# Kernel optimization log

Measured on AMD Instinct MI355X. Metric: run time of the kernel, lower is better.

## Reference

```python
import jax, jax.numpy as jnp
import numpy as np


def _build_affine_mat(affine, scale, translate, shear):
    """Replicates the torch stacking exactly: torch.stack(cols, dim=2) makes each
    stacked 3-vector a COLUMN of the 3x3 matrix."""
    tx, ty, tz = affine[:, 0], affine[:, 1], affine[:, 2]
    sx, sy, sz = scale[:, 0], scale[:, 1], scale[:, 2]
    trx, try_, trz = translate[:, 0], translate[:, 1], translate[:, 2]
    sh_xy, sh_xz, sh_yx, sh_yz, sh_zx, sh_zy = (shear[:, i] for i in range(6))
    one = jnp.ones_like(tx)
    zero = jnp.zeros_like(tx)

    col = lambda a, b, c: jnp.stack([a, b, c], axis=1)          # [N,3]
    mat3 = lambda c0, c1, c2: jnp.stack([c0, c1, c2], axis=2)   # columns -> [N,3,3]

    rot_x = mat3(col(one, zero, zero),
                 col(zero, jnp.cos(tx), -jnp.sin(tx)),
                 col(zero, jnp.sin(tx), jnp.cos(tx)))
    rot_y = mat3(col(jnp.cos(ty), zero, jnp.sin(ty)),
                 col(zero, one, zero),
                 col(-jnp.sin(ty), zero, jnp.cos(ty)))
    rot_z = mat3(col(jnp.cos(tz), -jnp.sin(tz), zero),
                 col(jnp.sin(tz), jnp.cos(tz), zero),
                 col(zero, zero, one))
    scale_mat = mat3(col(sx, zero, zero), col(zero, sy, zero), col(zero, zero, sz))
    shear_mat = mat3(col(one, jnp.tan(sh_xy), jnp.tan(sh_xz)),
                     col(jnp.tan(sh_yx), one, jnp.tan(sh_yz)),
                     col(jnp.tan(sh_zx), jnp.tan(sh_zy), one))
    trans = jnp.stack([trx, try_, trz], axis=1)[:, :, None]     # [N,3,1]

    m = shear_mat @ (scale_mat @ (rot_z @ (rot_y @ rot_x)))     # [N,3,3]
    return jnp.concatenate([m, trans], axis=-1)                 # [N,3,4]


def _affine_grid_3d(mat, D, H, W):
    """F.affine_grid(mat, [N,C,D,H,W], align_corners=True): grid[n,d,h,w] =
    mat @ (x_w, y_h, z_d, 1), coords in torch (x,y,z) = (W,H,D) order."""
    xs = jnp.linspace(-1.0, 1.0, W)
    ys = jnp.linspace(-1.0, 1.0, H)
    zs = jnp.linspace(-1.0, 1.0, D)
    zz, yy, xx = jnp.meshgrid(zs, ys, xs, indexing='ij')        # each [D,H,W]
    base = jnp.stack([xx, yy, zz], axis=-1)                     # [D,H,W,3]
    grid = jnp.einsum('dhwj,nij->ndhwi', base, mat[:, :, :3])
    return grid + mat[:, None, None, None, :, 3]                # [N,D,H,W,3]


def _grid_sample_3d(src, grid):
    """F.grid_sample(src, grid, mode='bilinear', padding_mode='zeros',
    align_corners=True) for 5-D input."""
    N, C, D, H, W = src.shape
    x, y, z = grid[..., 0], grid[..., 1], grid[..., 2]
    ix = (x + 1.0) * 0.5 * (W - 1)
    iy = (y + 1.0) * 0.5 * (H - 1)
    iz = (z + 1.0) * 0.5 * (D - 1)
    fx, fy, fz = jnp.floor(ix), jnp.floor(iy), jnp.floor(iz)
    wx, wy, wz = ix - fx, iy - fy, iz - fz                      # frac weights
    x0, y0, z0 = fx.astype(jnp.int32), fy.astype(jnp.int32), fz.astype(jnp.int32)

    gather = jax.vmap(lambda im, zi, yi, xi: im[:, zi, yi, xi])  # [C,D,H,W] per batch

    out = jnp.zeros((N, C, D, H, W), dtype=src.dtype)
    for dz in (0, 1):
        for dy in (0, 1):
            for dx in (0, 1):
                xi, yi, zi = x0 + dx, y0 + dy, z0 + dz
                w = ((wx if dx else 1.0 - wx) *
                     (wy if dy else 1.0 - wy) *
                     (wz if dz else 1.0 - wz))
                valid = ((xi >= 0) & (xi < W) & (yi >= 0) & (yi < H) &
                         (zi >= 0) & (zi < D))
                xc = jnp.clip(xi, 0, W - 1)
                yc = jnp.clip(yi, 0, H - 1)
                zc = jnp.clip(zi, 0, D - 1)
                g = gather(src, zc, yc, xc)                      # [N,C,D,H,W]
                out = out + (w * valid)[:, None] * g
    return out


def setup_inputs() -> dict:
    key = jax.random.key(0)
    k = jax.random.split(key, 5)
    N, C, D, H, W = 2, 1, 160, 192, 160
    src = jax.random.normal(k[0], (N, C, D, H, W), dtype=jnp.float32)
    affine = 0.1 * jax.random.normal(k[1], (N, 3), dtype=jnp.float32)
    scale = 1.0 + 0.05 * jax.random.normal(k[2], (N, 3), dtype=jnp.float32)
    translate = 0.05 * jax.random.normal(k[3], (N, 3), dtype=jnp.float32)
    shear = 0.05 * jax.random.normal(k[4], (N, 6), dtype=jnp.float32)
    return {"src": src, "affine": affine, "scale": scale,
            "translate": translate, "shear": shear}


def reference(src, affine, scale, translate, shear):
    mat = _build_affine_mat(affine, scale, translate, shear)     # [N,3,4]
    N, C, D, H, W = src.shape
    grid = _affine_grid_3d(mat, D, H, W)                         # [N,D,H,W,3]
    out = _grid_sample_3d(src, grid)                             # [N,C,D,H,W]
    return out, mat
```

## Files before the change

kernel.cpp:

```cpp
#include <hip/hip_runtime.h>
#include <math.h>

#define N_ 2
#define C_ 1
#define D_ 160
#define H_ 192
#define W_ 160
#define DHW_ (D_*H_*W_)
#define TOTAL_ (N_*DHW_)
#define BLOCKS_PER_N_ (DHW_/256)

__device__ __forceinline__ void matmul3(const float A[3][3], const float B[3][3], float C[3][3]) {
    #pragma unroll
    for (int i = 0; i < 3; ++i)
        #pragma unroll
        for (int j = 0; j < 3; ++j)
            C[i][j] = A[i][0]*B[0][j] + A[i][1]*B[1][j] + A[i][2]*B[2][j];
}

__global__ void build_mat_kernel(const float* __restrict__ affine,
                                 const float* __restrict__ scale,
                                 const float* __restrict__ translate,
                                 const float* __restrict__ shear,
                                 float* __restrict__ mat_out) {
    int n = threadIdx.x;
    if (n >= N_) return;
    float tx = affine[n*3+0], ty = affine[n*3+1], tz = affine[n*3+2];
    float sx = scale[n*3+0],  sy = scale[n*3+1],  sz = scale[n*3+2];
    float t_xy = tanf(shear[n*6+0]), t_xz = tanf(shear[n*6+1]);
    float t_yx = tanf(shear[n*6+2]), t_yz = tanf(shear[n*6+3]);
    float t_zx = tanf(shear[n*6+4]), t_zy = tanf(shear[n*6+5]);
    float cx = cosf(tx), sxv = sinf(tx);
    float cy = cosf(ty), syv = sinf(ty);
    float cz = cosf(tz), szv = sinf(tz);
    float RX[3][3] = {{1,0,0},{0,cx,sxv},{0,-sxv,cx}};
    float RY[3][3] = {{cy,0,-syv},{0,1,0},{syv,0,cy}};
    float RZ[3][3] = {{cz,szv,0},{-szv,cz,0},{0,0,1}};
    float SC[3][3] = {{sx,0,0},{0,sy,0},{0,0,sz}};
    float SH[3][3] = {{1,t_yx,t_zx},{t_xy,1,t_zy},{t_xz,t_yz,1}};
    float M1[3][3], M2[3][3], M3[3][3], M4[3][3];
    matmul3(RY, RX, M1);
    matmul3(RZ, M1, M2);
    matmul3(SC, M2, M3);
    matmul3(SH, M3, M4);
    #pragma unroll
    for (int i = 0; i < 3; ++i) {
        #pragma unroll
        for (int j = 0; j < 3; ++j)
            mat_out[n*12 + i*4 + j] = M4[i][j];
        mat_out[n*12 + i*4 + 3] = translate[n*3 + i];
    }
}

__global__ __launch_bounds__(256)
void affine_sample_kernel(const float* __restrict__ src,
                          const float* __restrict__ mat,
                          float* __restrict__ out) {
    int n     = blockIdx.x / BLOCKS_PER_N_;
    int local = (blockIdx.x % BLOCKS_PER_N_) * 256 + threadIdx.x;

    int w = local % W_;
    int t = local / W_;
    int h = t % H_;
    int d = t / H_;

    const float* m = mat + n * 12;

    float x = -1.0f + w * (2.0f / (W_ - 1));
    float y = -1.0f + h * (2.0f / (H_ - 1));
    float z = -1.0f + d * (2.0f / (D_ - 1));

    float gx = m[0]*x + m[1]*y + m[2]*z  + m[3];
    float gy = m[4]*x + m[5]*y + m[6]*z  + m[7];
    float gz = m[8]*x + m[9]*y + m[10]*z + m[11];

    float ix = (gx + 1.0f) * 0.5f * (W_ - 1);
    float iy = (gy + 1.0f) * 0.5f * (H_ - 1);
    float iz = (gz + 1.0f) * 0.5f * (D_ - 1);

    float fx = floorf(ix), fy = floorf(iy), fz = floorf(iz);
    float wx = ix - fx, wy = iy - fy, wz = iz - fz;
    int x0 = (int)fx, y0 = (int)fy, z0 = (int)fz;

    const float* s = src + n * DHW_;
    float acc = 0.0f;
    #pragma unroll
    for (int dz = 0; dz < 2; ++dz) {
        int  zi  = z0 + dz;
        bool vz  = (zi >= 0) & (zi < D_);
        int  zc  = min(max(zi, 0), D_ - 1);
        float wzz = dz ? wz : 1.0f - wz;
        #pragma unroll
        for (int dy = 0; dy < 2; ++dy) {
            int  yi  = y0 + dy;
            bool vzy = vz & (yi >= 0) & (yi < H_);
            int  yc  = min(max(yi, 0), H_ - 1);
            float wzy = wzz * (dy ? wy : 1.0f - wy);
            int rowoff = (zc * H_ + yc) * W_;
            #pragma unroll
            for (int dx = 0; dx < 2; ++dx) {
                int  xi = x0 + dx;
                bool v  = vzy & (xi >= 0) & (xi < W_);
                int  xc = min(max(xi, 0), W_ - 1);
                float ww = wzy * (dx ? wx : 1.0f - wx);
                float val = v ? s[rowoff + xc] : 0.0f;
                acc += ww * val;
            }
        }
    }
    out[n * DHW_ + local] = acc;
}

extern "C" void kernel_launch(void* const* d_in, const int* in_sizes, int n_in,
                              void* d_out, int out_size, void* d_ws, size_t ws_size,
                              hipStream_t stream) {
    const float* src       = (const float*)d_in[0];
    const float* affine    = (const float*)d_in[1];
    const float* scale     = (const float*)d_in[2];
    const float* translate = (const float*)d_in[3];
    const float* shear     = (const float*)d_in[4];

    float* out     = (float*)d_out;
    float* mat_out = out + TOTAL_;

    build_mat_kernel<<<1, 64, 0, stream>>>(affine, scale, translate, shear, mat_out);
    affine_sample_kernel<<<N_ * BLOCKS_PER_N_, 256, 0, stream>>>(src, mat_out, out);
}
```

Before: 148.6 us.

## Process four voxels per thread with interior fast path and XCD-aware block swizzle

Each thread now computes four consecutive output voxels, hoisting the y/z part of the affine transform and storing results with one float4 write. A wave-uniform fast path skips per-corner bounds checks and clamps when every voxel's eight neighbours are in range, using lerp-form trilinear interpolation. Block IDs are remapped so consecutive work chunks land on the same XCD, which is meant to improve L2 locality of the gathered source reads. Register pressure rises, and boundary waves still run the slow masked path.

```diff
diff --git a/kernel.cpp b/kernel.cpp
--- a/kernel.cpp
+++ b/kernel.cpp
@@ -2,13 +2,18 @@
 #include <math.h>
 
 #define N_ 2
-#define C_ 1
 #define D_ 160
 #define H_ 192
 #define W_ 160
+#define HW_ (H_*W_)
 #define DHW_ (D_*H_*W_)
 #define TOTAL_ (N_*DHW_)
-#define BLOCKS_PER_N_ (DHW_/256)
+#define VPT_ 4
+#define BLK_ 256
+#define ELEMS_PER_BLK_ (BLK_*VPT_)
+#define BLOCKS_PER_N_ (DHW_/ELEMS_PER_BLK_)
+#define NWG_ (TOTAL_/ELEMS_PER_BLK_)
+#define NXCD_ 8
 
 __device__ __forceinline__ void matmul3(const float A[3][3], const float B[3][3], float C[3][3]) {
     #pragma unroll
@@ -56,59 +61,100 @@
 void affine_sample_kernel(const float* __restrict__ src,
                           const float* __restrict__ mat,
                           float* __restrict__ out) {
-    int n     = blockIdx.x / BLOCKS_PER_N_;
-    int local = (blockIdx.x % BLOCKS_PER_N_) * 256 + threadIdx.x;
+    int bid = blockIdx.x;
+    int swz = (bid & (NXCD_-1)) * (NWG_/NXCD_) + (bid >> 3);
 
-    int w = local % W_;
-    int t = local / W_;
-    int h = t % H_;
-    int d = t / H_;
+    int n  = swz / BLOCKS_PER_N_;
+    int lb = (swz % BLOCKS_PER_N_) * ELEMS_PER_BLK_ + threadIdx.x * VPT_;
+
+    int w0 = lb % W_;
+    int t  = lb / W_;
+    int h  = t % H_;
+    int d  = t / H_;
 
     const float* m = mat + n * 12;
-
-    float x = -1.0f + w * (2.0f / (W_ - 1));
     float y = -1.0f + h * (2.0f / (H_ - 1));
     float z = -1.0f + d * (2.0f / (D_ - 1));
+    float byx = m[1]*y + m[2]*z  + m[3];
+    float byy = m[5]*y + m[6]*z  + m[7];
+    float byz = m[9]*y + m[10]*z + m[11];
 
-    float gx = m[0]*x + m[1]*y + m[2]*z  + m[3];
-    float gy = m[4]*x + m[5]*y + m[6]*z  + m[7];
-    float gz = m[8]*x + m[9]*y + m[10]*z + m[11];
-
-    float ix = (gx + 1.0f) * 0.5f * (W_ - 1);
-    float iy = (gy + 1.0f) * 0.5f * (H_ - 1);
-    float iz = (gz + 1.0f) * 0.5f * (D_ - 1);
-
-    float fx = floorf(ix), fy = floorf(iy), fz = floorf(iz);
-    float wx = ix - fx, wy = iy - fy, wz = iz - fz;
-    int x0 = (int)fx, y0 = (int)fy, z0 = (int)fz;
+    int   x0[VPT_], y0[VPT_], z0[VPT_], off[VPT_];
+    float wx[VPT_], wy[VPT_], wz[VPT_];
+    bool  allin = true;
+    #pragma unroll
+    for (int k = 0; k < VPT_; ++k) {
+        float x  = -1.0f + (w0 + k) * (2.0f / (W_ - 1));
+        float ix = (m[0]*x + byx + 1.0f) * 0.5f * (W_ - 1);
+        float iy = (m[4]*x + byy + 1.0f) * 0.5f * (H_ - 1);
+        float iz = (m[8]*x + byz + 1.0f) * 0.5f * (D_ - 1);
+        float fx = floorf(ix), fy = floorf(iy), fz = floorf(iz);
+        wx[k] = ix - fx; wy[k] = iy - fy; wz[k] = iz - fz;
+        x0[k] = (int)fx; y0[k] = (int)fy; z0[k] = (int)fz;
+        off[k] = (z0[k] * H_ + y0[k]) * W_ + x0[k];
+        allin &= ((unsigned)x0[k] < (unsigned)(W_-1)) &
+                 ((unsigned)y0[k] < (unsigned)(H_-1)) &
+                 ((unsigned)z0[k] < (unsigned)(D_-1));
+    }
 
     const float* s = src + n * DHW_;
-    float acc = 0.0f;
-    #pragma unroll
-    for (int dz = 0; dz < 2; ++dz) {
-        int  zi  = z0 + dz;
-        bool vz  = (zi >= 0) & (zi < D_);
-        int  zc  = min(max(zi, 0), D_ - 1);
-        float wzz = dz ? wz : 1.0f - wz;
+    float res[VPT_];
+
+    if (__all(allin)) {
+        float v000[VPT_], v001[VPT_], v010[VPT_], v011[VPT_];
+        float v100[VPT_], v101[VPT_], v110[VPT_], v111[VPT_];
         #pragma unroll
-        for (int dy = 0; dy < 2; ++dy) {
-            int  yi  = y0 + dy;
-            bool vzy = vz & (yi >= 0) & (yi < H_);
-            int  yc  = min(max(yi, 0), H_ - 1);
-            float wzy = wzz * (dy ? wy : 1.0f - wy);
-            int rowoff = (zc * H_ + yc) * W_;
+        for (int k = 0; k < VPT_; ++k) {
+            const float* p = s + off[k];
+            v000[k] = p[0];        v001[k] = p[1];
+            v010[k] = p[W_];       v011[k] = p[W_ + 1];
+            v100[k] = p[HW_];      v101[k] = p[HW_ + 1];
+            v110[k] = p[HW_ + W_]; v111[k] = p[HW_ + W_ + 1];
+        }
+        #pragma unroll
+        for (int k = 0; k < VPT_; ++k) {
+            float c00 = v000[k] + wx[k] * (v001[k] - v000[k]);
+            float c01 = v010[k] + wx[k] * (v011[k] - v010[k]);
+            float c10 = v100[k] + wx[k] * (v101[k] - v100[k]);
+            float c11 = v110[k] + wx[k] * (v111[k] - v110[k]);
+            float c0  = c00 + wy[k] * (c01 - c00);
+            float c1  = c10 + wy[k] * (c11 - c10);
+            res[k] = c0 + wz[k] * (c1 - c0);
+        }
+    } else {
+        #pragma unroll
+        for (int k = 0; k < VPT_; ++k) {
+            float acc = 0.0f;
             #pragma unroll
-            for (int dx = 0; dx < 2; ++dx) {
-                int  xi = x0 + dx;
-                bool v  = vzy & (xi >= 0) & (xi < W_);
-                int  xc = min(max(xi, 0), W_ - 1);
-                float ww = wzy * (dx ? wx : 1.0f - wx);
-                float val = v ? s[rowoff + xc] : 0.0f;
-                acc += ww * val;
+            for (int dz = 0; dz < 2; ++dz) {
+                int  zi  = z0[k] + dz;
+                bool vz  = (zi >= 0) & (zi < D_);
+                int  zc  = min(max(zi, 0), D_ - 1);
+                float wzz = dz ? wz[k] : 1.0f - wz[k];
+                #pragma unroll
+                for (int dy = 0; dy < 2; ++dy) {
+                    int  yi  = y0[k] + dy;
+                    bool vzy = vz & (yi >= 0) & (yi < H_);
+                    int  yc  = min(max(yi, 0), H_ - 1);
+                    float wzy = wzz * (dy ? wy[k] : 1.0f - wy[k]);
+                    int rowoff = (zc * H_ + yc) * W_;
+                    #pragma unroll
+                    for (int dx = 0; dx < 2; ++dx) {
+                        int  xi = x0[k] + dx;
+                        bool v  = vzy & (xi >= 0) & (xi < W_);
+                        int  xc = min(max(xi, 0), W_ - 1);
+                        float ww = wzy * (dx ? wx[k] : 1.0f - wx[k]);
+                        float val = v ? s[rowoff + xc] : 0.0f;
+                        acc += ww * val;
+                    }
+                }
             }
+            res[k] = acc;
         }
     }
-    out[n * DHW_ + local] = acc;
+
+    float4 o = make_float4(res[0], res[1], res[2], res[3]);
+    *reinterpret_cast<float4*>(out + n * DHW_ + lb) = o;
 }
 
 extern "C" void kernel_launch(void* const* d_in, const int* in_sizes, int n_in,
@@ -124,5 +170,5 @@
     float* mat_out = out + TOTAL_;
 
     build_mat_kernel<<<1, 64, 0, stream>>>(affine, scale, translate, shear, mat_out);
-    affine_sample_kernel<<<N_ * BLOCKS_PER_N_, 256, 0, stream>>>(src, mat_out, out);
+    affine_sample_kernel<<<NWG_, BLK_, 0, stream>>>(src, mat_out, out);
 }
```

Result: slower. 201.0 us (+35.2%).

## Fuse matrix build into sampler, two depth slices per thread, XCD-aware block swizzle

Applied to the files above, without the earlier changes.

Drops the separate matrix-building kernel. Each block now computes the 3x4 affine matrix into shared memory, and block 0 writes both matrices to the output. Each thread handles two adjacent depth slices, issues all 16 gathers before doing any arithmetic, and uses branchless mask-multiplied lerps. Block indices are remapped so that consecutive work lands on the same XCD, which is meant to improve L2 locality. The cost is redundant transcendental math per block and higher register pressure.

```diff
diff --git a/kernel.cpp b/kernel.cpp
--- a/kernel.cpp
+++ b/kernel.cpp
@@ -2,13 +2,18 @@
 #include <math.h>
 
 #define N_ 2
-#define C_ 1
 #define D_ 160
 #define H_ 192
 #define W_ 160
+#define HW_ (H_*W_)
 #define DHW_ (D_*H_*W_)
 #define TOTAL_ (N_*DHW_)
-#define BLOCKS_PER_N_ (DHW_/256)
+#define BLK_ 256
+#define BLOCKS_PER_SLAB_ (HW_/BLK_)
+#define PAIRS_ (D_/2)
+#define BLOCKS_PER_N_ (PAIRS_*BLOCKS_PER_SLAB_)
+#define NWG_ (N_*BLOCKS_PER_N_)
+#define NXCD_ 8
 
 __device__ __forceinline__ void matmul3(const float A[3][3], const float B[3][3], float C[3][3]) {
     #pragma unroll
@@ -18,13 +23,10 @@
             C[i][j] = A[i][0]*B[0][j] + A[i][1]*B[1][j] + A[i][2]*B[2][j];
 }
 
-__global__ void build_mat_kernel(const float* __restrict__ affine,
-                                 const float* __restrict__ scale,
-                                 const float* __restrict__ translate,
-                                 const float* __restrict__ shear,
-                                 float* __restrict__ mat_out) {
-    int n = threadIdx.x;
-    if (n >= N_) return;
+__device__ __forceinline__ void compute_mat(int n,
+        const float* __restrict__ affine, const float* __restrict__ scale,
+        const float* __restrict__ translate, const float* __restrict__ shear,
+        float M[12]) {
     float tx = affine[n*3+0], ty = affine[n*3+1], tz = affine[n*3+2];
     float sx = scale[n*3+0],  sy = scale[n*3+1],  sz = scale[n*3+2];
     float t_xy = tanf(shear[n*6+0]), t_xz = tanf(shear[n*6+1]);
@@ -47,68 +49,120 @@
     for (int i = 0; i < 3; ++i) {
         #pragma unroll
         for (int j = 0; j < 3; ++j)
-            mat_out[n*12 + i*4 + j] = M4[i][j];
-        mat_out[n*12 + i*4 + 3] = translate[n*3 + i];
+            M[i*4+j] = M4[i][j];
+        M[i*4+3] = translate[n*3+i];
     }
 }
 
 __global__ __launch_bounds__(256)
 void affine_sample_kernel(const float* __restrict__ src,
-                          const float* __restrict__ mat,
-                          float* __restrict__ out) {
-    int n     = blockIdx.x / BLOCKS_PER_N_;
-    int local = (blockIdx.x % BLOCKS_PER_N_) * 256 + threadIdx.x;
+                          const float* __restrict__ affine,
+                          const float* __restrict__ scale,
+                          const float* __restrict__ translate,
+                          const float* __restrict__ shear,
+                          float* __restrict__ out,
+                          float* __restrict__ mat_out) {
+    int bid = blockIdx.x;
+    int swz = (bid & (NXCD_-1)) * (NWG_/NXCD_) + (bid >> 3);
 
-    int w = local % W_;
-    int t = local / W_;
-    int h = t % H_;
-    int d = t / H_;
+    int n = swz / BLOCKS_PER_N_;
+    int r = swz % BLOCKS_PER_N_;
 
-    const float* m = mat + n * 12;
+    __shared__ float sm[12];
+    if (threadIdx.x == 0) {
+        float M[12];
+        compute_mat(n, affine, scale, translate, shear, M);
+        #pragma unroll
+        for (int i = 0; i < 12; ++i) sm[i] = M[i];
+        if (bid == 0) {
+            #pragma unroll
+            for (int i = 0; i < 12; ++i) mat_out[i] = M[i];
+        }
+    }
+    if (bid == 0 && threadIdx.x == 1) {
+        float M[12];
+        compute_mat(1, affine, scale, translate, shear, M);
+        #pragma unroll
+        for (int i = 0; i < 12; ++i) mat_out[12 + i] = M[i];
+    }
+    __syncthreads();
 
-    float x = -1.0f + w * (2.0f / (W_ - 1));
-    float y = -1.0f + h * (2.0f / (H_ - 1));
-    float z = -1.0f + d * (2.0f / (D_ - 1));
+    int d0  = 2 * (r / BLOCKS_PER_SLAB_);
+    int idx = (r % BLOCKS_PER_SLAB_) * BLK_ + threadIdx.x;
+    int w = idx % W_;
+    int h = idx / W_;
 
-    float gx = m[0]*x + m[1]*y + m[2]*z  + m[3];
-    float gy = m[4]*x + m[5]*y + m[6]*z  + m[7];
-    float gz = m[8]*x + m[9]*y + m[10]*z + m[11];
+    float x = -1.0f + w  * (2.0f / (W_ - 1));
+    float y = -1.0f + h  * (2.0f / (H_ - 1));
+    float z = -1.0f + d0 * (2.0f / (D_ - 1));
 
-    float ix = (gx + 1.0f) * 0.5f * (W_ - 1);
-    float iy = (gy + 1.0f) * 0.5f * (H_ - 1);
-    float iz = (gz + 1.0f) * 0.5f * (D_ - 1);
+    float gx = sm[0]*x + sm[1]*y + sm[2]*z  + sm[3];
+    float gy = sm[4]*x + sm[5]*y + sm[6]*z  + sm[7];
+    float gz = sm[8]*x + sm[9]*y + sm[10]*z + sm[11];
 
-    float fx = floorf(ix), fy = floorf(iy), fz = floorf(iz);
-    float wx = ix - fx, wy = iy - fy, wz = iz - fz;
-    int x0 = (int)fx, y0 = (int)fy, z0 = (int)fz;
+    float ix[2], iy[2], iz[2];
+    ix[0] = (gx + 1.0f) * (0.5f * (W_ - 1));
+    iy[0] = (gy + 1.0f) * (0.5f * (H_ - 1));
+    iz[0] = (gz + 1.0f) * (0.5f * (D_ - 1));
+    const float zs = 2.0f / (D_ - 1);
+    ix[1] = ix[0] + sm[2]  * zs * (0.5f * (W_ - 1));
+    iy[1] = iy[0] + sm[6]  * zs * (0.5f * (H_ - 1));
+    iz[1] = iz[0] + sm[10] * zs * (0.5f * (D_ - 1));
+
+    float wxa[2], wya[2], wza[2];
+    float mx0[2], mx1[2], my0[2], my1[2], mz0[2], mz1[2];
+    int   r00[2], r01[2], r10[2], r11[2], xa0[2], xa1[2];
+    #pragma unroll
+    for (int k = 0; k < 2; ++k) {
+        float fx = floorf(ix[k]), fy = floorf(iy[k]), fz = floorf(iz[k]);
+        wxa[k] = ix[k] - fx; wya[k] = iy[k] - fy; wza[k] = iz[k] - fz;
+        int x0 = (int)fx, y0 = (int)fy, z0 = (int)fz;
+        int x1 = x0 + 1,  y1 = y0 + 1,  z1 = z0 + 1;
+        mx0[k] = ((unsigned)x0 < (unsigned)W_) ? 1.0f : 0.0f;
+        mx1[k] = ((unsigned)x1 < (unsigned)W_) ? 1.0f : 0.0f;
+        my0[k] = ((unsigned)y0 < (unsigned)H_) ? 1.0f : 0.0f;
+        my1[k] = ((unsigned)y1 < (unsigned)H_) ? 1.0f : 0.0f;
+        mz0[k] = ((unsigned)z0 < (unsigned)D_) ? 1.0f : 0.0f;
+        mz1[k] = ((unsigned)z1 < (unsigned)D_) ? 1.0f : 0.0f;
+        int xc0 = min(max(x0, 0), W_-1), xc1 = min(max(x1, 0), W_-1);
+        int yc0 = min(max(y0, 0), H_-1), yc1 = min(max(y1, 0), H_-1);
+        int zc0 = min(max(z0, 0), D_-1), zc1 = min(max(z1, 0), D_-1);
+        r00[k] = (zc0 * H_ + yc0) * W_;
+        r01[k] = (zc0 * H_ + yc1) * W_;
+        r10[k] = (zc1 * H_ + yc0) * W_;
+        r11[k] = (zc1 * H_ + yc1) * W_;
+        xa0[k] = xc0; xa1[k] = xc1;
+    }
 
     const float* s = src + n * DHW_;
-    float acc = 0.0f;
+    float v000[2], v001[2], v010[2], v011[2], v100[2], v101[2], v110[2], v111[2];
     #pragma unroll
-    for (int dz = 0; dz < 2; ++dz) {
-        int  zi  = z0 + dz;
-        bool vz  = (zi >= 0) & (zi < D_);
-        int  zc  = min(max(zi, 0), D_ - 1);
-        float wzz = dz ? wz : 1.0f - wz;
-        #pragma unroll
-        for (int dy = 0; dy < 2; ++dy) {
-            int  yi  = y0 + dy;
-            bool vzy = vz & (yi >= 0) & (yi < H_);
-            int  yc  = min(max(yi, 0), H_ - 1);
-            float wzy = wzz * (dy ? wy : 1.0f - wy);
-            int rowoff = (zc * H_ + yc) * W_;
-            #pragma unroll
-            for (int dx = 0; dx < 2; ++dx) {
-                int  xi = x0 + dx;
-                bool v  = vzy & (xi >= 0) & (xi < W_);
-                int  xc = min(max(xi, 0), W_ - 1);
-                float ww = wzy * (dx ? wx : 1.0f - wx);
-                float val = v ? s[rowoff + xc] : 0.0f;
-                acc += ww * val;
-            }
-        }
+    for (int k = 0; k < 2; ++k) {
+        v000[k] = s[r00[k] + xa0[k]]; v001[k] = s[r00[k] + xa1[k]];
+        v010[k] = s[r01[k] + xa0[k]]; v011[k] = s[r01[k] + xa1[k]];
+        v100[k] = s[r10[k] + xa0[k]]; v101[k] = s[r10[k] + xa1[k]];
+        v110[k] = s[r11[k] + xa0[k]]; v111[k] = s[r11[k] + xa1[k]];
     }
-    out[n * DHW_ + local] = acc;
+
+    float res[2];
+    #pragma unroll
+    for (int k = 0; k < 2; ++k) {
+        float a, b, c00, c01, c10, c11, c0, c1;
+        a = v000[k]*mx0[k]; b = v001[k]*mx1[k]; c00 = a + wxa[k]*(b - a);
+        a = v010[k]*mx0[k]; b = v011[k]*mx1[k]; c01 = a + wxa[k]*(b - a);
+        a = v100[k]*mx0[k]; b = v101[k]*mx1[k]; c10 = a + wxa[k]*(b - a);
+        a = v110[k]*mx0[k]; b = v111[k]*mx1[k]; c11 = a + wxa[k]*(b - a);
+        c00 *= my0[k]; c01 *= my1[k];
+        c10 *= my0[k]; c11 *= my1[k];
+        c0 = c00 + wya[k]*(c01 - c00);
+        c1 = c10 + wya[k]*(c11 - c10);
+        c0 *= mz0[k]; c1 *= mz1[k];
+        res[k] = c0 + wza[k]*(c1 - c0);
+    }
+
+    int obase = n * DHW_ + d0 * HW_ + idx;
+    out[obase]       = res[0];
+    out[obase + HW_] = res[1];
 }
 
 extern "C" void kernel_launch(void* const* d_in, const int* in_sizes, int n_in,
@@ -123,6 +177,6 @@
     float* out     = (float*)d_out;
     float* mat_out = out + TOTAL_;
 
-    build_mat_kernel<<<1, 64, 0, stream>>>(affine, scale, translate, shear, mat_out);
-    affine_sample_kernel<<<N_ * BLOCKS_PER_N_, 256, 0, stream>>>(src, mat_out, out);
+    affine_sample_kernel<<<NWG_, BLK_, 0, stream>>>(src, affine, scale, translate,
+                                                    shear, out, mat_out);
 }
```

Result: slower. 159.2 us (+7.1%).

## Swizzle blocks across XCDs and use branchless paired-load trilinear gather

Applied to the files above, without the earlier changes.

Remaps block IDs so that consecutive blocks land on the same XCD, which should improve L2 locality of the gathered source voxels on MI355X's multi-XCD layout. Replaces the predicated eight-way gather with four row pointers built from a clamped x base. Each row is read with two unconditional inline-asm global loads at offsets 0 and 4 bytes. Out-of-range taps are handled by select and mask multiplies, and the interpolation becomes a lerp chain. This removes branches and per-tap address math, but always loads from the clamped memory location and forces a full vmcnt(0) wait inside the asm.

```diff
diff --git a/kernel.cpp b/kernel.cpp
--- a/kernel.cpp
+++ b/kernel.cpp
@@ -2,13 +2,15 @@
 #include <math.h>
 
 #define N_ 2
-#define C_ 1
 #define D_ 160
 #define H_ 192
 #define W_ 160
+#define HW_ (H_*W_)
 #define DHW_ (D_*H_*W_)
 #define TOTAL_ (N_*DHW_)
 #define BLOCKS_PER_N_ (DHW_/256)
+#define NWG_ (TOTAL_/256)
+#define NXCD_ 8
 
 __device__ __forceinline__ void matmul3(const float A[3][3], const float B[3][3], float C[3][3]) {
     #pragma unroll
@@ -56,8 +58,11 @@
 void affine_sample_kernel(const float* __restrict__ src,
                           const float* __restrict__ mat,
                           float* __restrict__ out) {
-    int n     = blockIdx.x / BLOCKS_PER_N_;
-    int local = (blockIdx.x % BLOCKS_PER_N_) * 256 + threadIdx.x;
+    int bid = blockIdx.x;
+    int swz = (bid & (NXCD_-1)) * (NWG_/NXCD_) + (bid >> 3);
+
+    int n     = swz / BLOCKS_PER_N_;
+    int local = (swz % BLOCKS_PER_N_) * 256 + threadIdx.x;
 
     int w = local % W_;
     int t = local / W_;
@@ -74,40 +79,64 @@
     float gy = m[4]*x + m[5]*y + m[6]*z  + m[7];
     float gz = m[8]*x + m[9]*y + m[10]*z + m[11];
 
-    float ix = (gx + 1.0f) * 0.5f * (W_ - 1);
-    float iy = (gy + 1.0f) * 0.5f * (H_ - 1);
-    float iz = (gz + 1.0f) * 0.5f * (D_ - 1);
+    float ix = (gx + 1.0f) * (0.5f * (W_ - 1));
+    float iy = (gy + 1.0f) * (0.5f * (H_ - 1));
+    float iz = (gz + 1.0f) * (0.5f * (D_ - 1));
 
     float fx = floorf(ix), fy = floorf(iy), fz = floorf(iz);
     float wx = ix - fx, wy = iy - fy, wz = iz - fz;
     int x0 = (int)fx, y0 = (int)fy, z0 = (int)fz;
 
+    float mx0 = ((unsigned)(x0    ) < (unsigned)W_) ? 1.0f : 0.0f;
+    float mx1 = ((unsigned)(x0 + 1) < (unsigned)W_) ? 1.0f : 0.0f;
+    float my0 = ((unsigned)(y0    ) < (unsigned)H_) ? 1.0f : 0.0f;
+    float my1 = ((unsigned)(y0 + 1) < (unsigned)H_) ? 1.0f : 0.0f;
+    float mz0 = ((unsigned)(z0    ) < (unsigned)D_) ? 1.0f : 0.0f;
+    float mz1 = ((unsigned)(z0 + 1) < (unsigned)D_) ? 1.0f : 0.0f;
+
+    int xbase = min(max(x0, 0), W_ - 2);
+    int yc0 = min(max(y0,     0), H_ - 1), yc1 = min(max(y0 + 1, 0), H_ - 1);
+    int zc0 = min(max(z0,     0), D_ - 1), zc1 = min(max(z0 + 1, 0), D_ - 1);
+
     const float* s = src + n * DHW_;
-    float acc = 0.0f;
-    #pragma unroll
-    for (int dz = 0; dz < 2; ++dz) {
-        int  zi  = z0 + dz;
-        bool vz  = (zi >= 0) & (zi < D_);
-        int  zc  = min(max(zi, 0), D_ - 1);
-        float wzz = dz ? wz : 1.0f - wz;
-        #pragma unroll
-        for (int dy = 0; dy < 2; ++dy) {
-            int  yi  = y0 + dy;
-            bool vzy = vz & (yi >= 0) & (yi < H_);
-            int  yc  = min(max(yi, 0), H_ - 1);
-            float wzy = wzz * (dy ? wy : 1.0f - wy);
-            int rowoff = (zc * H_ + yc) * W_;
-            #pragma unroll
-            for (int dx = 0; dx < 2; ++dx) {
-                int  xi = x0 + dx;
-                bool v  = vzy & (xi >= 0) & (xi < W_);
-                int  xc = min(max(xi, 0), W_ - 1);
-                float ww = wzy * (dx ? wx : 1.0f - wx);
-                float val = v ? s[rowoff + xc] : 0.0f;
-                acc += ww * val;
-            }
-        }
-    }
+    const float* pr00 = s + (zc0 * H_ + yc0) * W_ + xbase;
+    const float* pr01 = s + (zc0 * H_ + yc1) * W_ + xbase;
+    const float* pr10 = s + (zc1 * H_ + yc0) * W_ + xbase;
+    const float* pr11 = s + (zc1 * H_ + yc1) * W_ + xbase;
+
+    float l00, h00, l01, h01, l10, h10, l11, h11;
+    asm volatile(
+        "global_load_dword %0, %8, off\n\t"
+        "global_load_dword %1, %8, off offset:4\n\t"
+        "global_load_dword %2, %9, off\n\t"
+        "global_load_dword %3, %9, off offset:4\n\t"
+        "global_load_dword %4, %10, off\n\t"
+        "global_load_dword %5, %10, off offset:4\n\t"
+        "global_load_dword %6, %11, off\n\t"
+        "global_load_dword %7, %11, off offset:4\n\t"
+        "s_waitcnt vmcnt(0)"
+        : "=&v"(l00), "=&v"(h00), "=&v"(l01), "=&v"(h01),
+          "=&v"(l10), "=&v"(h10), "=&v"(l11), "=&v"(h11)
+        : "v"(pr00), "v"(pr01), "v"(pr10), "v"(pr11));
+
+    bool selHi = (x0 > W_ - 2);
+    bool selLo = (x0 < 0);
+    float v000 = selHi ? h00 : l00,  v001 = selLo ? l00 : h00;
+    float v010 = selHi ? h01 : l01,  v011 = selLo ? l01 : h01;
+    float v100 = selHi ? h10 : l10,  v101 = selLo ? l10 : h10;
+    float v110 = selHi ? h11 : l11,  v111 = selLo ? l11 : h11;
+
+    float a, b;
+    a = v000 * mx0; b = v001 * mx1; float c00 = a + wx * (b - a);
+    a = v010 * mx0; b = v011 * mx1; float c01 = a + wx * (b - a);
+    a = v100 * mx0; b = v101 * mx1; float c10 = a + wx * (b - a);
+    a = v110 * mx0; b = v111 * mx1; float c11 = a + wx * (b - a);
+    c00 *= my0; c01 *= my1; c10 *= my0; c11 *= my1;
+    float c0 = c00 + wy * (c01 - c00);
+    float c1 = c10 + wy * (c11 - c10);
+    c0 *= mz0; c1 *= mz1;
+    float acc = c0 + wz * (c1 - c0);
+
     out[n * DHW_ + local] = acc;
 }
 
@@ -124,5 +153,5 @@
     float* mat_out = out + TOTAL_;
 
     build_mat_kernel<<<1, 64, 0, stream>>>(affine, scale, translate, shear, mat_out);
-    affine_sample_kernel<<<N_ * BLOCKS_PER_N_, 256, 0, stream>>>(src, mat_out, out);
+    affine_sample_kernel<<<NWG_, 256, 0, stream>>>(src, mat_out, out);
 }
```

After: 161.2 us. 1.08x slower.
